# Kernel tuning notes

Measured on AMD Instinct MI355X. Metric: run time of the kernel, lower is better.

## Reference

```python
import jax, jax.numpy as jnp
import numpy as np

B, S, D, H = 2, 2048, 1024, 16
HD = D // H  # head_dim = 64


def setup_inputs() -> dict:
    key = jax.random.key(0)
    ks = jax.random.split(key, 11)
    init = 1.0 / np.sqrt(D)
    inp = {
        "query": jax.random.normal(ks[0], (B, S, D), jnp.float32),
        "key": jax.random.normal(ks[1], (B, S, D), jnp.float32),
        "value": jax.random.normal(ks[2], (B, S, D), jnp.float32),
        "Wq": jax.random.uniform(ks[3], (D, D), jnp.float32, -init, init),
        "bq": jax.random.uniform(ks[4], (D,), jnp.float32, -init, init),
        "Wk": jax.random.uniform(ks[5], (D, D), jnp.float32, -init, init),
        "bk": jax.random.uniform(ks[6], (D,), jnp.float32, -init, init),
        "Wv": jax.random.uniform(ks[7], (D, D), jnp.float32, -init, init),
        "bv": jax.random.uniform(ks[8], (D,), jnp.float32, -init, init),
        "Wo": jax.random.uniform(ks[9], (D, D), jnp.float32, -init, init),
        "bo": jax.random.uniform(ks[10], (D,), jnp.float32, -init, init),
    }
    return inp


def reference(query, key, value, Wq, bq, Wk, bk, Wv, bv, Wo, bo):
    # Linear projections (torch Linear: x @ W.T + b)
    q = query @ Wq.T + bq  # [B,S,D]
    k = key @ Wk.T + bk
    v = value @ Wv.T + bv
    # split heads -> [B,H,S,HD]
    q = q.reshape(B, S, H, HD).transpose(0, 2, 1, 3)
    k = k.reshape(B, S, H, HD).transpose(0, 2, 1, 3)
    v = v.reshape(B, S, H, HD).transpose(0, 2, 1, 3)
    # NOTE: original code divides by scale = head_dim**-0.5, i.e. multiplies
    # scores by sqrt(head_dim). Reproduced faithfully.
    scale = HD ** (-0.5)
    scores = jnp.einsum("bhqd,bhkd->bhqk", q, k) / scale  # [B,H,S,S]
    attn = jax.nn.softmax(scores, axis=-1)
    x = jnp.einsum("bhqk,bhkd->bhqd", attn, v)  # [B,H,S,HD]
    x = x.transpose(0, 2, 1, 3).reshape(B, S, D)
    return x @ Wo.T + bo
```

## Files before the change

kernel.cpp:

```cpp
#include <hip/hip_runtime.h>
#include <stdint.h>
#include <stddef.h>

#define SCALE_LOG2E 11.541560327111707f
#define E8 4194304
#define M1 1048576

typedef __attribute__((ext_vector_type(8))) _Float16 f16x8;
typedef __attribute__((ext_vector_type(4))) _Float16 f16x4;
typedef __attribute__((ext_vector_type(4))) float f32x4;

#if __has_builtin(__builtin_amdgcn_exp2f)
#define EXP2F(x) __builtin_amdgcn_exp2f(x)
#else
#define EXP2F(x) exp2f(x)
#endif

__device__ __forceinline__ f32x4 mfma_f16(f16x8 a, f16x8 b, f32x4 c) {
  return __builtin_amdgcn_mfma_f32_16x16x32_f16(a, b, c, 0, 0, 0);
}

__device__ __forceinline__ void async16(const void* g, void* lds) {
  __builtin_amdgcn_global_load_lds(
      (const __attribute__((address_space(1))) unsigned int*)g,
      (__attribute__((address_space(3))) unsigned int*)lds, 16, 0, 0);
}

__global__ void prep_all(const float* __restrict__ q, const float* __restrict__ k,
                         const float* __restrict__ v,
                         const float* __restrict__ wq, const float* __restrict__ wk,
                         const float* __restrict__ wv, const float* __restrict__ wo,
                         _Float16* __restrict__ Xf, _Float16* __restrict__ Wf) {
  const int gid = blockIdx.x;
  const float* src;
  _Float16* dst;
  int i;
  if (gid < 12288) {
    const int z = gid >> 12;
    src = (z == 0) ? q : (z == 1) ? k : v;
    dst = Xf + (size_t)z * E8;
    i = (gid & 4095) * 256 + threadIdx.x;
  } else {
    const int g2 = gid - 12288;
    const int z = g2 >> 10;
    src = (z == 0) ? wq : (z == 1) ? wk : (z == 2) ? wv : wo;
    dst = Wf + (size_t)z * M1;
    i = (g2 & 1023) * 256 + threadIdx.x;
  }
  float4 x = ((const float4*)src)[i];
  f16x4 h = {(_Float16)x.x, (_Float16)x.y, (_Float16)x.z, (_Float16)x.w};
  ((f16x4*)dst)[i] = h;
}

__global__ __launch_bounds__(256, 3) void gemm_qkv(
    const _Float16* __restrict__ Xf,
    const _Float16* __restrict__ Wf,
    const float* __restrict__ bq, const float* __restrict__ bk,
    const float* __restrict__ bv,
    _Float16* __restrict__ Of)
{
  __shared__ _Float16 LA[2][4096];
  __shared__ _Float16 LB[2][4096];
  const int z = blockIdx.z;
  const int tid = threadIdx.x;
  const int lane = tid & 63;
  const int wv = tid >> 6;
  const int wm = wv >> 1, wn = wv & 1;
  const int rl = lane & 15, qd = lane >> 4;
  const int m0 = blockIdx.y * 128, n0 = blockIdx.x * 128;

  const _Float16* A0 = Xf + (size_t)z * E8;
  const _Float16* W0 = Wf + (size_t)z * M1;
  const float* bias = (z == 0) ? bq : (z == 1) ? bk : bv;

  f32x4 acc[4][4];
#pragma unroll
  for (int i = 0; i < 4; i++)
#pragma unroll
    for (int j = 0; j < 4; j++) acc[i][j] = f32x4{0.f, 0.f, 0.f, 0.f};

  const int srow = wv * 32 + (lane >> 2);
  const int scol = (lane & 3) * 8;

  auto stage = [&](int k0, int buf) {
    const _Float16* ga = A0 + (size_t)(m0 + srow) * 1024 + k0 + scol;
    async16(ga, &LA[buf][wv * 1024]);
    async16(ga + 16 * 1024, &LA[buf][wv * 1024 + 512]);
    const _Float16* gb = W0 + (size_t)(n0 + srow) * 1024 + k0 + scol;
    async16(gb, &LB[buf][wv * 1024]);
    async16(gb + 16 * 1024, &LB[buf][wv * 1024 + 512]);
  };

  stage(0, 0);
  for (int t = 0; t < 32; t++) {
    const int buf = t & 1;
    __syncthreads();
    if (t + 1 < 32) stage((t + 1) * 32, buf ^ 1);
    f16x8 af[4], bfr[4];
#pragma unroll
    for (int i = 0; i < 4; i++) af[i] = *(const f16x8*)&LA[buf][(wm * 64 + i * 16 + rl) * 32 + qd * 8];
#pragma unroll
    for (int j = 0; j < 4; j++) bfr[j] = *(const f16x8*)&LB[buf][(wn * 64 + j * 16 + rl) * 32 + qd * 8];
#pragma unroll
    for (int i = 0; i < 4; i++)
#pragma unroll
      for (int j = 0; j < 4; j++) acc[i][j] = mfma_f16(af[i], bfr[j], acc[i][j]);
  }

  if (z == 2) {
#pragma unroll
    for (int j = 0; j < 4; j++) {
      const int nn = n0 + wn * 64 + j * 16 + rl;
      const float bj = bias[nn];
      const int hh = nn >> 6, e = nn & 63;
#pragma unroll
      for (int i = 0; i < 4; i++) {
        const int mm = m0 + wm * 64 + i * 16 + qd * 4;
        const int b = mm >> 11, s = mm & 2047;
        f16x4 pk = {(_Float16)(acc[i][j][0] + bj), (_Float16)(acc[i][j][1] + bj),
                    (_Float16)(acc[i][j][2] + bj), (_Float16)(acc[i][j][3] + bj)};
        *(f16x4*)(Of + 2 * (size_t)E8 + (((size_t)((b * 16 + hh) * 64 + e)) << 11) + s) = pk;
      }
    }
  } else {
    const float scl = (z == 0) ? SCALE_LOG2E : 1.0f;
    _Float16* base = Of + (size_t)z * E8;
#pragma unroll
    for (int j = 0; j < 4; j++) {
      const int nn = n0 + wn * 64 + j * 16 + rl;
      const float bj = bias[nn];
      const int hh = nn >> 6, e = nn & 63;
#pragma unroll
      for (int i = 0; i < 4; i++) {
        const int mm = m0 + wm * 64 + i * 16 + qd * 4;
        const int b = mm >> 11;
#pragma unroll
        for (int r = 0; r < 4; r++) {
          const int s = (mm + r) & 2047;
          base[((size_t)((b * 16 + hh) * 2048 + s) << 6) + e] =
              (_Float16)((acc[i][j][r] + bj) * scl);
        }
      }
    }
  }
}

__global__ __launch_bounds__(256, 3) void attn_kernel(
    const _Float16* __restrict__ Qb,
    const _Float16* __restrict__ Kb,
    const _Float16* __restrict__ Vt,
    _Float16* __restrict__ Xo)
{
  __shared__ _Float16 Ks[2][4096];
  __shared__ _Float16 Vs[2][4096];
  __shared__ _Float16 Ps[4][16][76];
  const int tid = threadIdx.x;
  const int lane = tid & 63;
  const int wv = tid >> 6;
  const int rl = lane & 15, qd = lane >> 4;
  const int bh = blockIdx.y;
  const int q0 = blockIdx.x * 64 + wv * 16;

  f16x8 qf[2];
#pragma unroll
  for (int kk = 0; kk < 2; kk++)
    qf[kk] = *(const f16x8*)(Qb + ((size_t)bh * 2048 + q0 + rl) * 64 + kk * 32 + qd * 8);

  float m_ = -1e30f, l_ = 0.f;
  f32x4 o[4];
#pragma unroll
  for (int jt = 0; jt < 4; jt++) o[jt] = f32x4{0.f, 0.f, 0.f, 0.f};

  auto stage = [&](int kv, int buf) {
#pragma unroll
    for (int it = 0; it < 2; it++) {
      const int cI = it * 256 + tid;
      const int row = cI >> 3;
      const int c = (cI & 7) ^ (row & 7);
      const int dst = (it * 256 + wv * 64) * 8;
      async16(Kb + ((size_t)bh * 2048 + kv + row) * 64 + c * 8, &Ks[buf][dst]);
      async16(Vt + ((size_t)bh * 64 + row) * 2048 + kv + c * 8, &Vs[buf][dst]);
    }
  };

  stage(0, 0);

  for (int t = 0; t < 32; t++) {
    const int buf = t & 1;
    __syncthreads();
    if (t + 1 < 32) stage((t + 1) * 64, buf ^ 1);

    f32x4 sc[4];
#pragma unroll
    for (int nt = 0; nt < 4; nt++) sc[nt] = f32x4{0.f, 0.f, 0.f, 0.f};
#pragma unroll
    for (int nt = 0; nt < 4; nt++) {
      const int ro = (nt * 16 + rl) * 64;
#pragma unroll
      for (int kk = 0; kk < 2; kk++) {
        const int cc = (((kk * 4 + qd) ^ (rl & 7)) << 3);
        f16x8 kh = *(const f16x8*)&Ks[buf][ro + cc];
        sc[nt] = mfma_f16(kh, qf[kk], sc[nt]);
      }
    }

    float mloc = sc[0][0];
#pragma unroll
    for (int nt = 0; nt < 4; nt++)
#pragma unroll
      for (int r = 0; r < 4; r++) mloc = fmaxf(mloc, sc[nt][r]);
    float mx = fmaxf(mloc, __shfl_xor(mloc, 16));
    mx = fmaxf(mx, __shfl_xor(mx, 32));
    float sm = 0.f;
#pragma unroll
    for (int nt = 0; nt < 4; nt++)
#pragma unroll
      for (int r = 0; r < 4; r++) {
        float p = EXP2F(sc[nt][r] - mloc);
        sc[nt][r] = p;
        sm += p;
      }
    const float mold = m_;
    const float mnew = fmaxf(mold, mx);
    m_ = mnew;
    const float cf = EXP2F(mloc - mnew);
    if (__any(mnew > mold)) {
      const float al = EXP2F(mold - mnew);
      l_ = l_ * al + sm * cf;
#pragma unroll
      for (int jt = 0; jt < 4; jt++)
#pragma unroll
        for (int r = 0; r < 4; r++) o[jt][r] *= al;
    } else {
      l_ += sm * cf;
    }

#pragma unroll
    for (int nt = 0; nt < 4; nt++) {
      f16x4 pk = {(_Float16)(sc[nt][0] * cf), (_Float16)(sc[nt][1] * cf),
                  (_Float16)(sc[nt][2] * cf), (_Float16)(sc[nt][3] * cf)};
      *(f16x4*)&Ps[wv][rl][nt * 16 + qd * 4] = pk;
    }

#pragma unroll
    for (int kk2 = 0; kk2 < 2; kk2++) {
      f16x8 pf = *(const f16x8*)&Ps[wv][rl][kk2 * 32 + qd * 8];
#pragma unroll
      for (int jt = 0; jt < 4; jt++) {
        const int cc = (((kk2 * 4 + qd) ^ (rl & 7)) << 3);
        f16x8 vv = *(const f16x8*)&Vs[buf][(jt * 16 + rl) * 64 + cc];
        o[jt] = mfma_f16(vv, pf, o[jt]);
      }
    }
  }

  float lt = l_ + __shfl_xor(l_, 16);
  lt += __shfl_xor(lt, 32);
  const float inv = 1.0f / lt;
  const int b = bh >> 4, hh = bh & 15;
  const int q = q0 + rl;
#pragma unroll
  for (int jt = 0; jt < 4; jt++) {
    f16x4 pk = {(_Float16)(o[jt][0] * inv), (_Float16)(o[jt][1] * inv),
                (_Float16)(o[jt][2] * inv), (_Float16)(o[jt][3] * inv)};
    *(f16x4*)(Xo + ((size_t)(b * 2048 + q)) * 1024 + hh * 64 + jt * 16 + qd * 4) = pk;
  }
}

__global__ __launch_bounds__(256, 2) void gemm_out(
    const _Float16* __restrict__ A0,
    const _Float16* __restrict__ W0,
    const float* __restrict__ bias,
    float* __restrict__ out)
{
  __shared__ _Float16 LA[2][2048];
  __shared__ _Float16 LB[2][4096];
  const int tid = threadIdx.x;
  const int lane = tid & 63;
  const int wv = tid >> 6;
  const int wm = wv >> 1, wn = wv & 1;
  const int rl = lane & 15, qd = lane >> 4;
  const int m0 = blockIdx.y * 64, n0 = blockIdx.x * 128;

  f32x4 acc[2][4];
#pragma unroll
  for (int i = 0; i < 2; i++)
#pragma unroll
    for (int j = 0; j < 4; j++) acc[i][j] = f32x4{0.f, 0.f, 0.f, 0.f};

  auto stage = [&](int k0, int buf) {
    {
      const int row = tid >> 2, c = tid & 3;
      async16(A0 + (size_t)(m0 + row) * 1024 + k0 + c * 8, &LA[buf][wv * 512]);
    }
#pragma unroll
    for (int it = 0; it < 2; it++) {
      const int cI = it * 256 + tid;
      const int row = cI >> 2, c = cI & 3;
      async16(W0 + (size_t)(n0 + row) * 1024 + k0 + c * 8,
              &LB[buf][it * 2048 + wv * 512]);
    }
  };

  stage(0, 0);
  for (int t = 0; t < 32; t++) {
    const int buf = t & 1;
    __syncthreads();
    if (t + 1 < 32) stage((t + 1) * 32, buf ^ 1);
    f16x8 af[2], bfr[4];
#pragma unroll
    for (int i = 0; i < 2; i++) af[i] = *(const f16x8*)&LA[buf][(wm * 32 + i * 16 + rl) * 32 + qd * 8];
#pragma unroll
    for (int j = 0; j < 4; j++) bfr[j] = *(const f16x8*)&LB[buf][(wn * 64 + j * 16 + rl) * 32 + qd * 8];
#pragma unroll
    for (int i = 0; i < 2; i++)
#pragma unroll
      for (int j = 0; j < 4; j++) acc[i][j] = mfma_f16(af[i], bfr[j], acc[i][j]);
  }

#pragma unroll
  for (int j = 0; j < 4; j++) {
    const int nn = n0 + wn * 64 + j * 16 + rl;
    const float bj = bias[nn];
#pragma unroll
    for (int i = 0; i < 2; i++) {
      const int mm = m0 + wm * 32 + i * 16 + qd * 4;
#pragma unroll
      for (int r = 0; r < 4; r++)
        out[(size_t)(mm + r) * 1024 + nn] = acc[i][j][r] + bj;
    }
  }
}

extern "C" void kernel_launch(void* const* d_in, const int* in_sizes, int n_in,
                              void* d_out, int out_size, void* d_ws, size_t ws_size,
                              hipStream_t stream) {
  const float* query = (const float*)d_in[0];
  const float* key   = (const float*)d_in[1];
  const float* value = (const float*)d_in[2];
  const float* Wq = (const float*)d_in[3];
  const float* bq = (const float*)d_in[4];
  const float* Wk = (const float*)d_in[5];
  const float* bk = (const float*)d_in[6];
  const float* Wv = (const float*)d_in[7];
  const float* bv = (const float*)d_in[8];
  const float* Wo = (const float*)d_in[9];
  const float* bo = (const float*)d_in[10];

  _Float16* ws = (_Float16*)d_ws;
  _Float16* Xf = ws;
  _Float16* Wf = ws + 3 * (size_t)E8;
  _Float16* Qh = Wf + 4 * (size_t)M1;
  _Float16* Kh = Qh + (size_t)E8;
  _Float16* Vt = Kh + (size_t)E8;
  _Float16* Xa = Vt + (size_t)E8;

  prep_all<<<16384, 256, 0, stream>>>(query, key, value, Wq, Wk, Wv, Wo, Xf, Wf);
  gemm_qkv<<<dim3(8, 32, 3), 256, 0, stream>>>(Xf, Wf, bq, bk, bv, Qh);
  attn_kernel<<<dim3(32, 32), 256, 0, stream>>>(Qh, Kh, Vt, Xa);
  gemm_out<<<dim3(8, 64), 256, 0, stream>>>(Xa, Wf + 3 * (size_t)M1, bo, (float*)d_out);
}
```

Measured before the change: 254.6 us.

## Split attention KV range in two, widen per-wave Q tile, stage QK epilogue via LDS

The attention kernel now has each wave handle 32 query rows instead of 16, so every K/V fragment read from LDS feeds two MFMAs. The KV sequence is split into two halves across blocks, and the total block count stays the same. Partial outputs and (max, sum) pairs go to fp32 scratch and are combined by a new merge kernel that writes the fp16 head-concatenated result. Separately, the Q/K projection epilogue now transposes through shared memory with an XOR swizzle so global stores are 16-byte vectors instead of scalar fp16 writes. This costs an extra launch, fp32 partial traffic of roughly 32MB written and read, and higher register pressure from the doubled accumulators.

```diff
diff --git a/kernel.cpp b/kernel.cpp
--- a/kernel.cpp
+++ b/kernel.cpp
@@ -5,6 +5,7 @@
 #define SCALE_LOG2E 11.541560327111707f
 #define E8 4194304
 #define M1 1048576
+#define NROW 65536
 
 typedef __attribute__((ext_vector_type(8))) _Float16 f16x8;
 typedef __attribute__((ext_vector_type(4))) _Float16 f16x4;
@@ -59,8 +60,9 @@
     const float* __restrict__ bv,
     _Float16* __restrict__ Of)
 {
-  __shared__ _Float16 LA[2][4096];
-  __shared__ _Float16 LB[2][4096];
+  __shared__ _Float16 SMEM[16384];
+  _Float16* LA = SMEM;
+  _Float16* LB = SMEM + 8192;
   const int z = blockIdx.z;
   const int tid = threadIdx.x;
   const int lane = tid & 63;
@@ -84,11 +86,11 @@
 
   auto stage = [&](int k0, int buf) {
     const _Float16* ga = A0 + (size_t)(m0 + srow) * 1024 + k0 + scol;
-    async16(ga, &LA[buf][wv * 1024]);
-    async16(ga + 16 * 1024, &LA[buf][wv * 1024 + 512]);
+    async16(ga, &LA[buf * 4096 + wv * 1024]);
+    async16(ga + 16 * 1024, &LA[buf * 4096 + wv * 1024 + 512]);
     const _Float16* gb = W0 + (size_t)(n0 + srow) * 1024 + k0 + scol;
-    async16(gb, &LB[buf][wv * 1024]);
-    async16(gb + 16 * 1024, &LB[buf][wv * 1024 + 512]);
+    async16(gb, &LB[buf * 4096 + wv * 1024]);
+    async16(gb + 16 * 1024, &LB[buf * 4096 + wv * 1024 + 512]);
   };
 
   stage(0, 0);
@@ -98,9 +100,9 @@
     if (t + 1 < 32) stage((t + 1) * 32, buf ^ 1);
     f16x8 af[4], bfr[4];
 #pragma unroll
-    for (int i = 0; i < 4; i++) af[i] = *(const f16x8*)&LA[buf][(wm * 64 + i * 16 + rl) * 32 + qd * 8];
-#pragma unroll
-    for (int j = 0; j < 4; j++) bfr[j] = *(const f16x8*)&LB[buf][(wn * 64 + j * 16 + rl) * 32 + qd * 8];
+    for (int i = 0; i < 4; i++) af[i] = *(const f16x8*)&LA[buf * 4096 + (wm * 64 + i * 16 + rl) * 32 + qd * 8];
+#pragma unroll
+    for (int j = 0; j < 4; j++) bfr[j] = *(const f16x8*)&LB[buf * 4096 + (wn * 64 + j * 16 + rl) * 32 + qd * 8];
 #pragma unroll
     for (int i = 0; i < 4; i++)
 #pragma unroll
@@ -125,22 +127,32 @@
   } else {
     const float scl = (z == 0) ? SCALE_LOG2E : 1.0f;
     _Float16* base = Of + (size_t)z * E8;
+    __syncthreads();
 #pragma unroll
     for (int j = 0; j < 4; j++) {
-      const int nn = n0 + wn * 64 + j * 16 + rl;
-      const float bj = bias[nn];
+      const int nl = wn * 64 + j * 16 + rl;
+      const float bj = bias[n0 + nl];
+#pragma unroll
+      for (int i = 0; i < 4; i++) {
+        const int ml = wm * 64 + i * 16 + qd * 4;
+        const int np = nl ^ (qd << 4);
+#pragma unroll
+        for (int r = 0; r < 4; r++)
+          SMEM[(ml + r) * 128 + np] = (_Float16)((acc[i][j][r] + bj) * scl);
+      }
+    }
+    __syncthreads();
+#pragma unroll
+    for (int it2 = 0; it2 < 8; it2++) {
+      const int m = (it2 * 256 + tid) >> 4;
+      const int col8 = (tid & 15) * 8;
+      const int np = col8 ^ (((m >> 2) & 3) << 4);
+      f16x8 vrow = *(const f16x8*)&SMEM[m * 128 + np];
+      const int sg = m0 + m;
+      const int b = sg >> 11, s = sg & 2047;
+      const int nn = n0 + col8;
       const int hh = nn >> 6, e = nn & 63;
-#pragma unroll
-      for (int i = 0; i < 4; i++) {
-        const int mm = m0 + wm * 64 + i * 16 + qd * 4;
-        const int b = mm >> 11;
-#pragma unroll
-        for (int r = 0; r < 4; r++) {
-          const int s = (mm + r) & 2047;
-          base[((size_t)((b * 16 + hh) * 2048 + s) << 6) + e] =
-              (_Float16)((acc[i][j][r] + bj) * scl);
-        }
-      }
+      *(f16x8*)(base + (((size_t)((b * 16 + hh) * 2048 + s)) << 6) + e) = vrow;
     }
   }
 }
@@ -149,27 +161,35 @@
     const _Float16* __restrict__ Qb,
     const _Float16* __restrict__ Kb,
     const _Float16* __restrict__ Vt,
-    _Float16* __restrict__ Xo)
+    float* __restrict__ Op,
+    float2* __restrict__ ML)
 {
   __shared__ _Float16 Ks[2][4096];
   __shared__ _Float16 Vs[2][4096];
-  __shared__ _Float16 Ps[4][16][76];
+  __shared__ _Float16 Ps[4][32][76];
   const int tid = threadIdx.x;
   const int lane = tid & 63;
   const int wv = tid >> 6;
   const int rl = lane & 15, qd = lane >> 4;
-  const int bh = blockIdx.y;
-  const int q0 = blockIdx.x * 64 + wv * 16;
-
-  f16x8 qf[2];
-#pragma unroll
-  for (int kk = 0; kk < 2; kk++)
-    qf[kk] = *(const f16x8*)(Qb + ((size_t)bh * 2048 + q0 + rl) * 64 + kk * 32 + qd * 8);
-
-  float m_ = -1e30f, l_ = 0.f;
-  f32x4 o[4];
-#pragma unroll
-  for (int jt = 0; jt < 4; jt++) o[jt] = f32x4{0.f, 0.f, 0.f, 0.f};
+  const int bh = blockIdx.z;
+  const int half = blockIdx.y;
+  const int kvb = half * 1024;
+  const int q0 = blockIdx.x * 128 + wv * 32;
+
+  f16x8 qf[2][2];
+#pragma unroll
+  for (int mt = 0; mt < 2; mt++)
+#pragma unroll
+    for (int kk = 0; kk < 2; kk++)
+      qf[mt][kk] = *(const f16x8*)(Qb + ((size_t)bh * 2048 + q0 + mt * 16 + rl) * 64 +
+                                   kk * 32 + qd * 8);
+
+  float m_[2] = {-1e30f, -1e30f}, l_[2] = {0.f, 0.f};
+  f32x4 o[2][4];
+#pragma unroll
+  for (int mt = 0; mt < 2; mt++)
+#pragma unroll
+    for (int jt = 0; jt < 4; jt++) o[mt][jt] = f32x4{0.f, 0.f, 0.f, 0.f};
 
   auto stage = [&](int kv, int buf) {
 #pragma unroll
@@ -183,16 +203,18 @@
     }
   };
 
-  stage(0, 0);
-
-  for (int t = 0; t < 32; t++) {
+  stage(kvb, 0);
+
+  for (int t = 0; t < 16; t++) {
     const int buf = t & 1;
     __syncthreads();
-    if (t + 1 < 32) stage((t + 1) * 64, buf ^ 1);
-
-    f32x4 sc[4];
-#pragma unroll
-    for (int nt = 0; nt < 4; nt++) sc[nt] = f32x4{0.f, 0.f, 0.f, 0.f};
+    if (t + 1 < 16) stage(kvb + (t + 1) * 64, buf ^ 1);
+
+    f32x4 sc[2][4];
+#pragma unroll
+    for (int mt = 0; mt < 2; mt++)
+#pragma unroll
+      for (int nt = 0; nt < 4; nt++) sc[mt][nt] = f32x4{0.f, 0.f, 0.f, 0.f};
 #pragma unroll
     for (int nt = 0; nt < 4; nt++) {
       const int ro = (nt * 16 + rl) * 64;
@@ -200,71 +222,103 @@
       for (int kk = 0; kk < 2; kk++) {
         const int cc = (((kk * 4 + qd) ^ (rl & 7)) << 3);
         f16x8 kh = *(const f16x8*)&Ks[buf][ro + cc];
-        sc[nt] = mfma_f16(kh, qf[kk], sc[nt]);
-      }
-    }
-
-    float mloc = sc[0][0];
-#pragma unroll
-    for (int nt = 0; nt < 4; nt++)
-#pragma unroll
-      for (int r = 0; r < 4; r++) mloc = fmaxf(mloc, sc[nt][r]);
-    float mx = fmaxf(mloc, __shfl_xor(mloc, 16));
-    mx = fmaxf(mx, __shfl_xor(mx, 32));
-    float sm = 0.f;
-#pragma unroll
-    for (int nt = 0; nt < 4; nt++)
-#pragma unroll
-      for (int r = 0; r < 4; r++) {
-        float p = EXP2F(sc[nt][r] - mloc);
-        sc[nt][r] = p;
-        sm += p;
-      }
-    const float mold = m_;
-    const float mnew = fmaxf(mold, mx);
-    m_ = mnew;
-    const float cf = EXP2F(mloc - mnew);
-    if (__any(mnew > mold)) {
-      const float al = EXP2F(mold - mnew);
-      l_ = l_ * al + sm * cf;
-#pragma unroll
-      for (int jt = 0; jt < 4; jt++)
-#pragma unroll
-        for (int r = 0; r < 4; r++) o[jt][r] *= al;
-    } else {
-      l_ += sm * cf;
-    }
-
-#pragma unroll
-    for (int nt = 0; nt < 4; nt++) {
-      f16x4 pk = {(_Float16)(sc[nt][0] * cf), (_Float16)(sc[nt][1] * cf),
-                  (_Float16)(sc[nt][2] * cf), (_Float16)(sc[nt][3] * cf)};
-      *(f16x4*)&Ps[wv][rl][nt * 16 + qd * 4] = pk;
+#pragma unroll
+        for (int mt = 0; mt < 2; mt++)
+          sc[mt][nt] = mfma_f16(kh, qf[mt][kk], sc[mt][nt]);
+      }
+    }
+
+#pragma unroll
+    for (int mt = 0; mt < 2; mt++) {
+      float mloc = sc[mt][0][0];
+#pragma unroll
+      for (int nt = 0; nt < 4; nt++)
+#pragma unroll
+        for (int r = 0; r < 4; r++) mloc = fmaxf(mloc, sc[mt][nt][r]);
+      float mx = fmaxf(mloc, __shfl_xor(mloc, 16));
+      mx = fmaxf(mx, __shfl_xor(mx, 32));
+      float sm = 0.f;
+#pragma unroll
+      for (int nt = 0; nt < 4; nt++)
+#pragma unroll
+        for (int r = 0; r < 4; r++) {
+          float p = EXP2F(sc[mt][nt][r] - mloc);
+          sc[mt][nt][r] = p;
+          sm += p;
+        }
+      const float mold = m_[mt];
+      const float mnew = fmaxf(mold, mx);
+      m_[mt] = mnew;
+      const float cf = EXP2F(mloc - mnew);
+      if (__any(mnew > mold)) {
+        const float al = EXP2F(mold - mnew);
+        l_[mt] = l_[mt] * al + sm * cf;
+#pragma unroll
+        for (int jt = 0; jt < 4; jt++)
+#pragma unroll
+          for (int r = 0; r < 4; r++) o[mt][jt][r] *= al;
+      } else {
+        l_[mt] += sm * cf;
+      }
+
+#pragma unroll
+      for (int nt = 0; nt < 4; nt++) {
+        f16x4 pk = {(_Float16)(sc[mt][nt][0] * cf), (_Float16)(sc[mt][nt][1] * cf),
+                    (_Float16)(sc[mt][nt][2] * cf), (_Float16)(sc[mt][nt][3] * cf)};
+        *(f16x4*)&Ps[wv][mt * 16 + rl][nt * 16 + qd * 4] = pk;
+      }
     }
 
 #pragma unroll
     for (int kk2 = 0; kk2 < 2; kk2++) {
-      f16x8 pf = *(const f16x8*)&Ps[wv][rl][kk2 * 32 + qd * 8];
+      f16x8 pf[2];
+#pragma unroll
+      for (int mt = 0; mt < 2; mt++)
+        pf[mt] = *(const f16x8*)&Ps[wv][mt * 16 + rl][kk2 * 32 + qd * 8];
 #pragma unroll
       for (int jt = 0; jt < 4; jt++) {
         const int cc = (((kk2 * 4 + qd) ^ (rl & 7)) << 3);
         f16x8 vv = *(const f16x8*)&Vs[buf][(jt * 16 + rl) * 64 + cc];
-        o[jt] = mfma_f16(vv, pf, o[jt]);
-      }
-    }
-  }
-
-  float lt = l_ + __shfl_xor(l_, 16);
-  lt += __shfl_xor(lt, 32);
-  const float inv = 1.0f / lt;
+#pragma unroll
+        for (int mt = 0; mt < 2; mt++)
+          o[mt][jt] = mfma_f16(vv, pf[mt], o[mt][jt]);
+      }
+    }
+  }
+
+#pragma unroll
+  for (int mt = 0; mt < 2; mt++) {
+    float lt = l_[mt] + __shfl_xor(l_[mt], 16);
+    lt += __shfl_xor(lt, 32);
+    const size_t row = (size_t)bh * 2048 + q0 + mt * 16 + rl;
+    float* op = Op + ((size_t)half * NROW + row) * 64;
+#pragma unroll
+    for (int jt = 0; jt < 4; jt++)
+      *(f32x4*)(op + jt * 16 + qd * 4) = o[mt][jt];
+    if (qd == 0) ML[(size_t)half * NROW + row] = make_float2(m_[mt], lt);
+  }
+}
+
+__global__ void merge_kernel(const float* __restrict__ Op,
+                             const float2* __restrict__ ML,
+                             _Float16* __restrict__ Xo) {
+  const int t = threadIdx.x;
+  const int row = blockIdx.x * 16 + (t >> 4);
+  const int d0 = (t & 15) * 4;
+  const float2 ml1 = ML[row];
+  const float2 ml2 = ML[NROW + row];
+  const float m = fmaxf(ml1.x, ml2.x);
+  const float w1 = EXP2F(ml1.x - m), w2 = EXP2F(ml2.x - m);
+  const float inv = 1.0f / (ml1.y * w1 + ml2.y * w2);
+  const float4 o1 = *(const float4*)(Op + (size_t)row * 64 + d0);
+  const float4 o2 = *(const float4*)(Op + (size_t)NROW * 64 + (size_t)row * 64 + d0);
+  const int bh = row >> 11, q = row & 2047;
   const int b = bh >> 4, hh = bh & 15;
-  const int q = q0 + rl;
-#pragma unroll
-  for (int jt = 0; jt < 4; jt++) {
-    f16x4 pk = {(_Float16)(o[jt][0] * inv), (_Float16)(o[jt][1] * inv),
-                (_Float16)(o[jt][2] * inv), (_Float16)(o[jt][3] * inv)};
-    *(f16x4*)(Xo + ((size_t)(b * 2048 + q)) * 1024 + hh * 64 + jt * 16 + qd * 4) = pk;
-  }
+  f16x4 pk = {(_Float16)((o1.x * w1 + o2.x * w2) * inv),
+              (_Float16)((o1.y * w1 + o2.y * w2) * inv),
+              (_Float16)((o1.z * w1 + o2.z * w2) * inv),
+              (_Float16)((o1.w * w1 + o2.w * w2) * inv)};
+  *(f16x4*)(Xo + ((size_t)(b * 2048 + q)) * 1024 + hh * 64 + d0) = pk;
 }
 
 __global__ __launch_bounds__(256, 2) void gemm_out(
@@ -354,9 +408,12 @@
   _Float16* Kh = Qh + (size_t)E8;
   _Float16* Vt = Kh + (size_t)E8;
   _Float16* Xa = Vt + (size_t)E8;
+  float*    Op = (float*)(Xa + (size_t)E8);
+  float2*   ML = (float2*)(Op + 2 * (size_t)NROW * 64);
 
   prep_all<<<16384, 256, 0, stream>>>(query, key, value, Wq, Wk, Wv, Wo, Xf, Wf);
   gemm_qkv<<<dim3(8, 32, 3), 256, 0, stream>>>(Xf, Wf, bq, bk, bv, Qh);
-  attn_kernel<<<dim3(32, 32), 256, 0, stream>>>(Qh, Kh, Vt, Xa);
+  attn_kernel<<<dim3(16, 2, 32), 256, 0, stream>>>(Qh, Kh, Vt, Op, ML);
+  merge_kernel<<<4096, 256, 0, stream>>>(Op, ML, Xa);
   gemm_out<<<dim3(8, 64), 256, 0, stream>>>(Xa, Wf + 3 * (size_t)M1, bo, (float*)d_out);
 }
```

Result: faster. 245.7 us (-3.5%).
